# Optimization experiments

Hardware: AMD Instinct MI355X
Metric: run time of the kernel (lower is better)

## Reference

```python
import jax, jax.numpy as jnp
import numpy as np

N = 10000      # nodes
E = 160000     # edges (before self-loops)
IN = 256
NEG_SLOPE = 0.2  # PyG GATConv default


def gat_layer(x, src, dst, W, a_src, a_dst, bias, heads, concat, n):
    # x: [n, in_dim]; W: [in_dim, heads*C]; a_src/a_dst: [heads, C]
    C = W.shape[1] // heads
    h = (x @ W).reshape(n, heads, C)                      # [n,H,C]
    es = jnp.einsum('nhc,hc->nh', h, a_src)               # [n,H]
    ed = jnp.einsum('nhc,hc->nh', h, a_dst)               # [n,H]
    e = jax.nn.leaky_relu(es[src] + ed[dst], NEG_SLOPE)   # [E,H]
    # segment softmax over destination node (every node has a self-loop)
    emax = jax.ops.segment_max(e, dst, num_segments=n)    # [n,H]
    al = jnp.exp(e - emax[dst])                           # [E,H]
    den = jax.ops.segment_sum(al, dst, num_segments=n)    # [n,H]
    al = al / den[dst]
    out = jax.ops.segment_sum(h[src] * al[:, :, None], dst, num_segments=n)  # [n,H,C]
    out = out.reshape(n, heads * C) if concat else out.mean(axis=1)
    return out + bias


def setup_inputs() -> dict:
    key = jax.random.key(0)
    ks = jax.random.split(key, 16)
    s = 0.05
    p = lambda k, shp: jax.random.normal(k, shp, dtype=jnp.float32) * s
    return {
        'x': jax.random.normal(ks[0], (N, IN), dtype=jnp.float32),
        'edge_index': jax.random.randint(ks[1], (2, E), 0, N, dtype=jnp.int64),
        'proj_w': p(ks[2], (IN, 512)), 'proj_b': jnp.zeros((512,), jnp.float32),
        'w1': p(ks[3], (512, 4 * 512)),  'as1': p(ks[4], (4, 512)), 'ad1': p(ks[5], (4, 512)),  'b1': jnp.zeros((2048,), jnp.float32),
        'w2': p(ks[6], (2048, 4 * 512)), 'as2': p(ks[7], (4, 512)), 'ad2': p(ks[8], (4, 512)),  'b2': jnp.zeros((2048,), jnp.float32),
        'w3': p(ks[9], (2048, 2 * 512)), 'as3': p(ks[10], (2, 512)), 'ad3': p(ks[11], (2, 512)), 'b3': jnp.zeros((512,), jnp.float32),
    }


def reference(x, edge_index, proj_w, proj_b, w1, as1, ad1, b1,
              w2, as2, ad2, b2, w3, as3, ad3, b3):
    n = x.shape[0]
    loops = jnp.arange(n, dtype=edge_index.dtype)
    src = jnp.concatenate([edge_index[0], loops])   # PyG add_self_loops=True
    dst = jnp.concatenate([edge_index[1], loops])
    h = x @ proj_w + proj_b                         # dropout is identity in eval
    h = gat_layer(h, src, dst, w1, as1, ad1, b1, 4, True, n)
    h = jax.nn.elu(h)
    h = gat_layer(h, src, dst, w2, as2, ad2, b2, 4, True, n)
    h = jax.nn.elu(h)
    h = gat_layer(h, src, dst, w3, as3, ad3, b3, 2, False, n)
    return h
```

## Files before the change

### kernel.cpp

```cpp
#include <hip/hip_runtime.h>
#include <hip/hip_bf16.h>
#include <math.h>

#define CDIV(a,b) (((a)+(b)-1)/(b))

typedef __bf16  bf16x8 __attribute__((ext_vector_type(8)));
typedef float   f32x4  __attribute__((ext_vector_type(4)));
typedef unsigned short u16x8 __attribute__((ext_vector_type(8)));
typedef unsigned short u16x4 __attribute__((ext_vector_type(4)));

__device__ __forceinline__ float bf2f(unsigned short u) {
    union { unsigned int i; float f; } x; x.i = ((unsigned int)u) << 16; return x.f;
}
__device__ __forceinline__ unsigned short f2bf(float f) {
    union { float f; unsigned int i; } x; x.f = f;
    unsigned int r = x.i + 0x7fff + ((x.i >> 16) & 1);
    return (unsigned short)(r >> 16);
}

__global__ void hist_kernel(const int* __restrict__ ei, int* __restrict__ deg,
                            int E, int Et) {
    int e = blockIdx.x * blockDim.x + threadIdx.x;
    if (e >= Et) return;
    int d = (e < E) ? ei[E + e] : (e - E);
    atomicAdd(&deg[d], 1);
}

__global__ void scan_kernel(const int* __restrict__ deg, int* __restrict__ off, int n) {
    __shared__ int buf[1024];
    __shared__ int carry_s;
    int t = threadIdx.x;
    if (t == 0) carry_s = 0;
    __syncthreads();
    for (int base = 0; base < n; base += 1024) {
        int v = (base + t < n) ? deg[base + t] : 0;
        buf[t] = v;
        __syncthreads();
        for (int s = 1; s < 1024; s <<= 1) {
            int x = (t >= s) ? buf[t - s] : 0;
            __syncthreads();
            buf[t] += x;
            __syncthreads();
        }
        int incl = buf[t];
        int carry = carry_s;
        __syncthreads();
        if (t == 1023) carry_s = carry + incl;
        if (base + t < n) off[base + t] = carry + incl - v;
        __syncthreads();
    }
    if (t == 0) off[n] = carry_s;
}

__global__ void scatter_kernel(const int* __restrict__ ei, const int* __restrict__ off,
                               int* __restrict__ cur, int* __restrict__ csr,
                               int E, int Et) {
    int e = blockIdx.x * blockDim.x + threadIdx.x;
    if (e >= Et) return;
    int s, d;
    if (e < E) { s = ei[e]; d = ei[E + e]; } else { s = e - E; d = s; }
    int pos = off[d] + atomicAdd(&cur[d], 1);
    csr[pos] = s;
}

__global__ void wt_transpose_kernel(const float* __restrict__ w,
                                    __hip_bfloat16* __restrict__ wt,
                                    int K, int N) {
    __shared__ float tile[32][33];
    int kb = blockIdx.x * 32, nb = blockIdx.y * 32;
    int tx = threadIdx.x & 31, ty = threadIdx.x >> 5;
    for (int i = ty; i < 32; i += 8)
        tile[i][tx] = w[(size_t)(kb + i) * N + nb + tx];
    __syncthreads();
    for (int i = ty; i < 32; i += 8)
        wt[(size_t)(nb + i) * K + kb + tx] = __float2bfloat16(tile[tx][i]);
}

__global__ void cvt_bf16_kernel(const float* __restrict__ in,
                                __hip_bfloat16* __restrict__ out, int total) {
    int i = blockIdx.x * blockDim.x + threadIdx.x;
    if (i < total) out[i] = __float2bfloat16(in[i]);
}

__device__ __forceinline__ void gload16(void* lds, const void* g) {
    __builtin_amdgcn_global_load_lds(
        (const __attribute__((address_space(1))) void*)g,
        (__attribute__((address_space(3))) void*)lds, 16, 0, 0);
}

__global__ __launch_bounds__(256) void gemm_bf16_kernel(
    const __hip_bfloat16* __restrict__ A,
    const __hip_bfloat16* __restrict__ BT,
    const float* __restrict__ bias,
    __hip_bfloat16* __restrict__ Cb,
    int M, int N, int K, int MB, int NB, int XT)
{
    __shared__ __align__(16) __hip_bfloat16 As[128 * 32];
    __shared__ __align__(16) __hip_bfloat16 Bs[128 * 32];

    const int bid  = blockIdx.x;
    const int xcd  = bid & 7;
    const int slot = bid >> 3;
    const int x_sub = slot / NB;
    const int yb    = slot - x_sub * NB;
    const int xb    = xcd * XT + x_sub;
    if (xb >= MB) return;

    const int tid = threadIdx.x;
    const int m0 = xb * 128, n0 = yb * 128;
    const int w = tid >> 6, l = tid & 63;
    const int wm = (w & 1) * 64, wn = (w >> 1) * 64;
    const int lm = l & 15, lq = l >> 4;

    f32x4 acc[4][4] = {};

    const int arow = tid >> 2;
    const int acol = (tid & 3) * 8;
    const __hip_bfloat16* Ag = A  + (size_t)(m0 + arow) * K + acol;
    const __hip_bfloat16* Bg = BT + (size_t)(n0 + arow) * K + acol;
    char* AsW = (char*)As + (w << 10);
    char* BsW = (char*)Bs + (w << 10);

    for (int k0 = 0; k0 < K; k0 += 32) {
        gload16(AsW,        Ag + k0);
        gload16(AsW + 4096, Ag + (size_t)64 * K + k0);
        gload16(BsW,        Bg + k0);
        gload16(BsW + 4096, Bg + (size_t)64 * K + k0);
        __syncthreads();
        bf16x8 af[4], bfr[4];
#pragma unroll
        for (int i = 0; i < 4; i++)
            af[i] = *(const bf16x8*)(As + (wm + i * 16 + lm) * 32 + lq * 8);
#pragma unroll
        for (int j = 0; j < 4; j++)
            bfr[j] = *(const bf16x8*)(Bs + (wn + j * 16 + lm) * 32 + lq * 8);
#pragma unroll
        for (int i = 0; i < 4; i++)
#pragma unroll
            for (int j = 0; j < 4; j++)
                acc[i][j] = __builtin_amdgcn_mfma_f32_16x16x32_bf16(
                    af[i], bfr[j], acc[i][j], 0, 0, 0);
        __syncthreads();
    }

#pragma unroll
    for (int i = 0; i < 4; i++) {
        int rb = m0 + wm + i * 16 + lq * 4;
#pragma unroll
        for (int r = 0; r < 4; r++) {
            int row = rb + r;
            if (row >= M) continue;
#pragma unroll
            for (int j = 0; j < 4; j++) {
                int col = n0 + wn + j * 16 + lm;
                float v = acc[i][j][r];
                if (bias) v += bias[col];
                Cb[(size_t)row * N + col] = __float2bfloat16(v);
            }
        }
    }
}

__global__ void esed_kernel(const __hip_bfloat16* __restrict__ h,
                            const float* __restrict__ a_src,
                            const float* __restrict__ a_dst,
                            float* __restrict__ es, float* __restrict__ ed, int H) {
    int nidx = blockIdx.x;
    int t = threadIdx.x;
    int head = t >> 6, lane = t & 63;
    const unsigned short* hp =
        (const unsigned short*)h + (size_t)nidx * H * 512 + head * 512 + lane * 8;
    const float* sp = a_src + head * 512 + lane * 8;
    const float* dp = a_dst + head * 512 + lane * 8;
    u16x8 hv = *(const u16x8*)hp;
    float4 s0 = *(const float4*)sp, s1 = *(const float4*)(sp + 4);
    float4 d0 = *(const float4*)dp, d1 = *(const float4*)(dp + 4);
    float hf[8];
#pragma unroll
    for (int k = 0; k < 8; k++) hf[k] = bf2f(hv[k]);
    float s = hf[0]*s0.x + hf[1]*s0.y + hf[2]*s0.z + hf[3]*s0.w
            + hf[4]*s1.x + hf[5]*s1.y + hf[6]*s1.z + hf[7]*s1.w;
    float d = hf[0]*d0.x + hf[1]*d0.y + hf[2]*d0.z + hf[3]*d0.w
            + hf[4]*d1.x + hf[5]*d1.y + hf[6]*d1.z + hf[7]*d1.w;
    for (int o = 32; o; o >>= 1) { s += __shfl_down(s, o); d += __shfl_down(d, o); }
    if (lane == 0) { es[nidx * H + head] = s; ed[nidx * H + head] = d; }
}

template<int H, int VEC, bool MEAN>
__global__ __launch_bounds__(256) void agg_kernel(
    const __hip_bfloat16* __restrict__ h, const float* __restrict__ es,
    const float* __restrict__ ed, const int* __restrict__ csr,
    const int* __restrict__ off, const float* __restrict__ bias,
    float* __restrict__ outF, __hip_bfloat16* __restrict__ outB, int do_elu)
{
    constexpr int HS = H * 512;
    __shared__ float red[MEAN ? 1024 : 1];
    int d = blockIdx.x, t = threadIdx.x;
    int c0 = t * VEC;
    int head = c0 >> 9;
    float edd = ed[d * H + head];
    int beg = off[d], end = off[d + 1];
    float acc[VEC];
#pragma unroll
    for (int k = 0; k < VEC; k++) acc[k] = 0.f;
    float den = 0.f;
    const unsigned short* hb = (const unsigned short*)h;

    int i = beg;
    for (; i + 1 < end; i += 2) {
        int s0 = csr[i], s1 = csr[i + 1];
        float e0 = es[s0 * H + head] + edd;
        float e1 = es[s1 * H + head] + edd;
        e0 = (e0 > 0.f) ? e0 : 0.2f * e0;
        e1 = (e1 > 0.f) ? e1 : 0.2f * e1;
        float w0 = __expf(e0), w1 = __expf(e1);
        den += w0 + w1;
        const unsigned short* hp0 = hb + (size_t)s0 * HS + c0;
        const unsigned short* hp1 = hb + (size_t)s1 * HS + c0;
        if constexpr (VEC == 8) {
            u16x8 v0 = *(const u16x8*)hp0;
            u16x8 v1 = *(const u16x8*)hp1;
#pragma unroll
            for (int k = 0; k < 8; k++) acc[k] = fmaf(w0, bf2f(v0[k]), acc[k]);
#pragma unroll
            for (int k = 0; k < 8; k++) acc[k] = fmaf(w1, bf2f(v1[k]), acc[k]);
        } else {
            u16x4 v0 = *(const u16x4*)hp0;
            u16x4 v1 = *(const u16x4*)hp1;
#pragma unroll
            for (int k = 0; k < VEC; k++) acc[k] = fmaf(w0, bf2f(v0[k]), acc[k]);
#pragma unroll
            for (int k = 0; k < VEC; k++) acc[k] = fmaf(w1, bf2f(v1[k]), acc[k]);
        }
    }
    if (i < end) {
        int s0 = csr[i];
        float e0 = es[s0 * H + head] + edd;
        e0 = (e0 > 0.f) ? e0 : 0.2f * e0;
        float w0 = __expf(e0);
        den += w0;
        const unsigned short* hp0 = hb + (size_t)s0 * HS + c0;
        if constexpr (VEC == 8) {
            u16x8 v0 = *(const u16x8*)hp0;
#pragma unroll
            for (int k = 0; k < 8; k++) acc[k] = fmaf(w0, bf2f(v0[k]), acc[k]);
        } else {
            u16x4 v0 = *(const u16x4*)hp0;
#pragma unroll
            for (int k = 0; k < VEC; k++) acc[k] = fmaf(w0, bf2f(v0[k]), acc[k]);
        }
    }

    float inv = 1.f / den;
    if constexpr (!MEAN) {
        u16x8 ov;
#pragma unroll
        for (int k = 0; k < VEC; k++) {
            float v = acc[k] * inv + bias[c0 + k];
            if (do_elu) v = (v > 0.f) ? v : expm1f(v);
            ov[k] = f2bf(v);
        }
        *(u16x8*)((unsigned short*)outB + (size_t)d * HS + c0) = ov;
    } else {
#pragma unroll
        for (int k = 0; k < VEC; k++) red[c0 + k] = acc[k] * inv;
        __syncthreads();
        if (t < 128) {
#pragma unroll
            for (int k = 0; k < 4; k++) {
                int c = t * 4 + k;
                outF[(size_t)d * 512 + c] = 0.5f * (red[c] + red[c + 512]) + bias[c];
            }
        }
    }
}

extern "C" void kernel_launch(void* const* d_in, const int* in_sizes, int n_in,
                              void* d_out, int out_size, void* d_ws, size_t ws_size,
                              hipStream_t stream) {
    const float* x      = (const float*)d_in[0];
    const int*   ei     = (const int*)  d_in[1];
    const float* proj_w = (const float*)d_in[2];
    const float* proj_b = (const float*)d_in[3];
    const float* w1  = (const float*)d_in[4];
    const float* as1 = (const float*)d_in[5];
    const float* ad1 = (const float*)d_in[6];
    const float* b1  = (const float*)d_in[7];
    const float* w2  = (const float*)d_in[8];
    const float* as2 = (const float*)d_in[9];
    const float* ad2 = (const float*)d_in[10];
    const float* b2  = (const float*)d_in[11];
    const float* w3  = (const float*)d_in[12];
    const float* as3 = (const float*)d_in[13];
    const float* ad3 = (const float*)d_in[14];
    const float* b3  = (const float*)d_in[15];

    const int n    = in_sizes[0] / 256;
    const int E    = in_sizes[1] / 2;
    const int Et   = E + n;
    const int MB   = CDIV(n, 128);
    const int Mpad = MB * 128;
    const int XT   = CDIV(MB, 8);

    char* p = (char*)d_ws;
    auto carve = [&](size_t bytes) {
        void* r = (void*)p;
        p += (bytes + 255) & ~(size_t)255;
        return r;
    };
    __hip_bfloat16* h_bf   = (__hip_bfloat16*)carve((size_t)Mpad * 2048 * sizeof(__hip_bfloat16));
    __hip_bfloat16* act_bf = (__hip_bfloat16*)carve((size_t)Mpad * 2048 * sizeof(__hip_bfloat16));
    __hip_bfloat16* x_bf   = (__hip_bfloat16*)carve((size_t)Mpad * 256 * sizeof(__hip_bfloat16));
    __hip_bfloat16* h0_bf  = (__hip_bfloat16*)carve((size_t)Mpad * 512 * sizeof(__hip_bfloat16));
    __hip_bfloat16* pwt    = (__hip_bfloat16*)carve((size_t)512 * 256 * sizeof(__hip_bfloat16));
    __hip_bfloat16* w1t    = (__hip_bfloat16*)carve((size_t)2048 * 512 * sizeof(__hip_bfloat16));
    __hip_bfloat16* w2t    = (__hip_bfloat16*)carve((size_t)2048 * 2048 * sizeof(__hip_bfloat16));
    __hip_bfloat16* w3t    = (__hip_bfloat16*)carve((size_t)1024 * 2048 * sizeof(__hip_bfloat16));
    float* es  = (float*)carve((size_t)n * 4 * sizeof(float));
    float* ed  = (float*)carve((size_t)n * 4 * sizeof(float));
    int* deg = (int*)carve((size_t)n * sizeof(int));
    int* cur = (int*)carve((size_t)n * sizeof(int));
    int* off = (int*)carve((size_t)(n + 1) * sizeof(int));
    int* csr = (int*)carve((size_t)Et * sizeof(int));
    (void)ws_size; (void)n_in;

    hipMemsetAsync(deg, 0, n * sizeof(int), stream);
    hipMemsetAsync(cur, 0, n * sizeof(int), stream);
    hist_kernel<<<CDIV(Et, 256), 256, 0, stream>>>(ei, deg, E, Et);
    scan_kernel<<<1, 1024, 0, stream>>>(deg, off, n);
    scatter_kernel<<<CDIV(Et, 256), 256, 0, stream>>>(ei, off, cur, csr, E, Et);

    wt_transpose_kernel<<<dim3(256 / 32, 512 / 32),  256, 0, stream>>>(proj_w, pwt, 256, 512);
    wt_transpose_kernel<<<dim3(512 / 32, 2048 / 32), 256, 0, stream>>>(w1, w1t, 512, 2048);
    wt_transpose_kernel<<<dim3(2048 / 32, 2048 / 32),256, 0, stream>>>(w2, w2t, 2048, 2048);
    wt_transpose_kernel<<<dim3(2048 / 32, 1024 / 32),256, 0, stream>>>(w3, w3t, 2048, 1024);
    cvt_bf16_kernel<<<CDIV(n * 256, 256), 256, 0, stream>>>(x, x_bf, n * 256);

    auto gemm_grid = [&](int NB) { return 8 * XT * NB; };

    gemm_bf16_kernel<<<gemm_grid(4), 256, 0, stream>>>(
        x_bf, pwt, proj_b, h0_bf, n, 512, 256, MB, 4, XT);

    gemm_bf16_kernel<<<gemm_grid(16), 256, 0, stream>>>(
        h0_bf, w1t, nullptr, h_bf, n, 2048, 512, MB, 16, XT);
    esed_kernel<<<n, 4 * 64, 0, stream>>>(h_bf, as1, ad1, es, ed, 4);
    agg_kernel<4, 8, false><<<n, 256, 0, stream>>>(h_bf, es, ed, csr, off, b1,
                                                   nullptr, act_bf, 1);

    gemm_bf16_kernel<<<gemm_grid(16), 256, 0, stream>>>(
        act_bf, w2t, nullptr, h_bf, n, 2048, 2048, MB, 16, XT);
    esed_kernel<<<n, 4 * 64, 0, stream>>>(h_bf, as2, ad2, es, ed, 4);
    agg_kernel<4, 8, false><<<n, 256, 0, stream>>>(h_bf, es, ed, csr, off, b2,
                                                   nullptr, act_bf, 1);

    gemm_bf16_kernel<<<gemm_grid(8), 256, 0, stream>>>(
        act_bf, w3t, nullptr, h_bf, n, 1024, 2048, MB, 8, XT);
    esed_kernel<<<n, 2 * 64, 0, stream>>>(h_bf, as3, ad3, es, ed, 2);
    agg_kernel<2, 4, true><<<n, 256, 0, stream>>>(h_bf, es, ed, csr, off, b3,
                                                  (float*)d_out, nullptr, 0);
}
```

Measured before the change: 676.7 us.

## Fold input projection into layer-1 weights, shuffle-based scan, unroll aggregation by four

Precomputes the combined weight (W1^T · proj_w^T) and effective bias proj_b·W1, so the first GEMM runs directly on x with K=256 instead of two GEMMs (x@proj_w, then @W1). This removes the projection GEMM and its intermediate buffer. It also replaces the LDS-based Hillis-Steele scan with wave shuffle scans, and unrolls the edge aggregation loop to four neighbors so more gathers are in flight. Folding the weights changes bf16 rounding: the combined weight is rounded once and the intermediate activations are no longer rounded.

```diff
diff --git a/kernel.cpp b/kernel.cpp
--- a/kernel.cpp
+++ b/kernel.cpp
@@ -27,26 +27,36 @@
 }
 
 __global__ void scan_kernel(const int* __restrict__ deg, int* __restrict__ off, int n) {
-    __shared__ int buf[1024];
+    __shared__ int wsum[16];
     __shared__ int carry_s;
-    int t = threadIdx.x;
+    int t = threadIdx.x, lane = t & 63, wv = t >> 6;
     if (t == 0) carry_s = 0;
     __syncthreads();
     for (int base = 0; base < n; base += 1024) {
         int v = (base + t < n) ? deg[base + t] : 0;
-        buf[t] = v;
-        __syncthreads();
-        for (int s = 1; s < 1024; s <<= 1) {
-            int x = (t >= s) ? buf[t - s] : 0;
-            __syncthreads();
-            buf[t] += x;
-            __syncthreads();
-        }
-        int incl = buf[t];
-        int carry = carry_s;
-        __syncthreads();
-        if (t == 1023) carry_s = carry + incl;
-        if (base + t < n) off[base + t] = carry + incl - v;
+        int x = v;
+#pragma unroll
+        for (int o = 1; o < 64; o <<= 1) {
+            int y = __shfl_up(x, o);
+            if (lane >= o) x += y;
+        }
+        if (lane == 63) wsum[wv] = x;
+        __syncthreads();
+        if (wv == 0 && lane < 16) {
+            int s = wsum[lane];
+#pragma unroll
+            for (int o = 1; o < 16; o <<= 1) {
+                int y = __shfl_up(s, o);
+                if (lane >= o) s += y;
+            }
+            wsum[lane] = s;
+        }
+        __syncthreads();
+        int wprev = (wv == 0) ? 0 : wsum[wv - 1];
+        int incl = carry_s + wprev + x;
+        if (base + t < n) off[base + t] = incl - v;
+        __syncthreads();
+        if (t == 1023) carry_s = incl;
         __syncthreads();
     }
     if (t == 0) off[n] = carry_s;
@@ -80,6 +90,15 @@
                                 __hip_bfloat16* __restrict__ out, int total) {
     int i = blockIdx.x * blockDim.x + threadIdx.x;
     if (i < total) out[i] = __float2bfloat16(in[i]);
+}
+
+__global__ void beff_kernel(const float* __restrict__ pb, const float* __restrict__ w1,
+                            float* __restrict__ beff, int K, int N) {
+    int j = blockIdx.x * blockDim.x + threadIdx.x;
+    if (j >= N) return;
+    float s = 0.f;
+    for (int k = 0; k < K; k++) s = fmaf(pb[k], w1[(size_t)k * N + j], s);
+    beff[j] = s;
 }
 
 __device__ __forceinline__ void gload16(void* lds, const void* g) {
@@ -207,33 +226,41 @@
     const unsigned short* hb = (const unsigned short*)h;
 
     int i = beg;
-    for (; i + 1 < end; i += 2) {
-        int s0 = csr[i], s1 = csr[i + 1];
-        float e0 = es[s0 * H + head] + edd;
-        float e1 = es[s1 * H + head] + edd;
-        e0 = (e0 > 0.f) ? e0 : 0.2f * e0;
-        e1 = (e1 > 0.f) ? e1 : 0.2f * e1;
-        float w0 = __expf(e0), w1 = __expf(e1);
-        den += w0 + w1;
-        const unsigned short* hp0 = hb + (size_t)s0 * HS + c0;
-        const unsigned short* hp1 = hb + (size_t)s1 * HS + c0;
+    for (; i + 3 < end; i += 4) {
+        int   s[4];
+        float wgt[4];
+#pragma unroll
+        for (int u = 0; u < 4; u++) {
+            s[u] = csr[i + u];
+            float e = es[s[u] * H + head] + edd;
+            e = (e > 0.f) ? e : 0.2f * e;
+            wgt[u] = __expf(e);
+        }
         if constexpr (VEC == 8) {
-            u16x8 v0 = *(const u16x8*)hp0;
-            u16x8 v1 = *(const u16x8*)hp1;
-#pragma unroll
-            for (int k = 0; k < 8; k++) acc[k] = fmaf(w0, bf2f(v0[k]), acc[k]);
-#pragma unroll
-            for (int k = 0; k < 8; k++) acc[k] = fmaf(w1, bf2f(v1[k]), acc[k]);
+            u16x8 v[4];
+#pragma unroll
+            for (int u = 0; u < 4; u++)
+                v[u] = *(const u16x8*)(hb + (size_t)s[u] * HS + c0);
+#pragma unroll
+            for (int u = 0; u < 4; u++) {
+                den += wgt[u];
+#pragma unroll
+                for (int k = 0; k < 8; k++) acc[k] = fmaf(wgt[u], bf2f(v[u][k]), acc[k]);
+            }
         } else {
-            u16x4 v0 = *(const u16x4*)hp0;
-            u16x4 v1 = *(const u16x4*)hp1;
-#pragma unroll
-            for (int k = 0; k < VEC; k++) acc[k] = fmaf(w0, bf2f(v0[k]), acc[k]);
-#pragma unroll
-            for (int k = 0; k < VEC; k++) acc[k] = fmaf(w1, bf2f(v1[k]), acc[k]);
-        }
-    }
-    if (i < end) {
+            u16x4 v[4];
+#pragma unroll
+            for (int u = 0; u < 4; u++)
+                v[u] = *(const u16x4*)(hb + (size_t)s[u] * HS + c0);
+#pragma unroll
+            for (int u = 0; u < 4; u++) {
+                den += wgt[u];
+#pragma unroll
+                for (int k = 0; k < VEC; k++) acc[k] = fmaf(wgt[u], bf2f(v[u][k]), acc[k]);
+            }
+        }
+    }
+    for (; i < end; i++) {
         int s0 = csr[i];
         float e0 = es[s0 * H + head] + edd;
         e0 = (e0 > 0.f) ? e0 : 0.2f * e0;
@@ -308,14 +335,15 @@
         p += (bytes + 255) & ~(size_t)255;
         return r;
     };
-    __hip_bfloat16* h_bf   = (__hip_bfloat16*)carve((size_t)Mpad * 2048 * sizeof(__hip_bfloat16));
-    __hip_bfloat16* act_bf = (__hip_bfloat16*)carve((size_t)Mpad * 2048 * sizeof(__hip_bfloat16));
-    __hip_bfloat16* x_bf   = (__hip_bfloat16*)carve((size_t)Mpad * 256 * sizeof(__hip_bfloat16));
-    __hip_bfloat16* h0_bf  = (__hip_bfloat16*)carve((size_t)Mpad * 512 * sizeof(__hip_bfloat16));
-    __hip_bfloat16* pwt    = (__hip_bfloat16*)carve((size_t)512 * 256 * sizeof(__hip_bfloat16));
-    __hip_bfloat16* w1t    = (__hip_bfloat16*)carve((size_t)2048 * 512 * sizeof(__hip_bfloat16));
-    __hip_bfloat16* w2t    = (__hip_bfloat16*)carve((size_t)2048 * 2048 * sizeof(__hip_bfloat16));
-    __hip_bfloat16* w3t    = (__hip_bfloat16*)carve((size_t)1024 * 2048 * sizeof(__hip_bfloat16));
+    __hip_bfloat16* h_bf    = (__hip_bfloat16*)carve((size_t)Mpad * 2048 * sizeof(__hip_bfloat16));
+    __hip_bfloat16* act_bf  = (__hip_bfloat16*)carve((size_t)Mpad * 2048 * sizeof(__hip_bfloat16));
+    __hip_bfloat16* x_bf    = (__hip_bfloat16*)carve((size_t)Mpad * 256 * sizeof(__hip_bfloat16));
+    __hip_bfloat16* pw_bf   = (__hip_bfloat16*)carve((size_t)256 * 512 * sizeof(__hip_bfloat16));
+    __hip_bfloat16* w1t     = (__hip_bfloat16*)carve((size_t)2048 * 512 * sizeof(__hip_bfloat16));
+    __hip_bfloat16* w2t     = (__hip_bfloat16*)carve((size_t)2048 * 2048 * sizeof(__hip_bfloat16));
+    __hip_bfloat16* w3t     = (__hip_bfloat16*)carve((size_t)1024 * 2048 * sizeof(__hip_bfloat16));
+    __hip_bfloat16* w_efft  = (__hip_bfloat16*)carve((size_t)2048 * 256 * sizeof(__hip_bfloat16));
+    float* b_eff = (float*)carve((size_t)2048 * sizeof(float));
     float* es  = (float*)carve((size_t)n * 4 * sizeof(float));
     float* ed  = (float*)carve((size_t)n * 4 * sizeof(float));
     int* deg = (int*)carve((size_t)n * sizeof(int));
@@ -330,19 +358,20 @@
     scan_kernel<<<1, 1024, 0, stream>>>(deg, off, n);
     scatter_kernel<<<CDIV(Et, 256), 256, 0, stream>>>(ei, off, cur, csr, E, Et);
 
-    wt_transpose_kernel<<<dim3(256 / 32, 512 / 32),  256, 0, stream>>>(proj_w, pwt, 256, 512);
     wt_transpose_kernel<<<dim3(512 / 32, 2048 / 32), 256, 0, stream>>>(w1, w1t, 512, 2048);
     wt_transpose_kernel<<<dim3(2048 / 32, 2048 / 32),256, 0, stream>>>(w2, w2t, 2048, 2048);
     wt_transpose_kernel<<<dim3(2048 / 32, 1024 / 32),256, 0, stream>>>(w3, w3t, 2048, 1024);
+    cvt_bf16_kernel<<<CDIV(256 * 512, 256), 256, 0, stream>>>(proj_w, pw_bf, 256 * 512);
     cvt_bf16_kernel<<<CDIV(n * 256, 256), 256, 0, stream>>>(x, x_bf, n * 256);
 
+    gemm_bf16_kernel<<<8 * 2 * 2, 256, 0, stream>>>(
+        w1t, pw_bf, nullptr, w_efft, 2048, 256, 512, 16, 2, 2);
+    beff_kernel<<<CDIV(2048, 256), 256, 0, stream>>>(proj_b, w1, b_eff, 512, 2048);
+
     auto gemm_grid = [&](int NB) { return 8 * XT * NB; };
 
-    gemm_bf16_kernel<<<gemm_grid(4), 256, 0, stream>>>(
-        x_bf, pwt, proj_b, h0_bf, n, 512, 256, MB, 4, XT);
-
     gemm_bf16_kernel<<<gemm_grid(16), 256, 0, stream>>>(
-        h0_bf, w1t, nullptr, h_bf, n, 2048, 512, MB, 16, XT);
+        x_bf, w_efft, b_eff, h_bf, n, 2048, 256, MB, 16, XT);
     esed_kernel<<<n, 4 * 64, 0, stream>>>(h_bf, as1, ad1, es, ed, 4);
     agg_kernel<4, 8, false><<<n, 256, 0, stream>>>(h_bf, es, ed, csr, off, b1,
                                                    nullptr, act_bf, 1);
```

New measurement: 777.0 us. +14.8%, slower.
